# Kernel optimization log

Hardware: AMD Instinct MI355X
Metric: run time of the kernel (lower is better)

Reference implementation:

```python
import jax, jax.numpy as jnp
import numpy as np

NUM_LUT, IN_F, OUT_F = 3, 4096, 4096
VEC, LUT, GROUP = 4, 16, 128
G = IN_F // VEC            # 1024 vector-groups along in_features
NG = IN_F // GROUP         # 32 quantization groups


def setup_inputs() -> dict:
    key = jax.random.key(0)
    k1, k2, k3, k4 = jax.random.split(key, 4)
    gate = jax.random.normal(k1, (NUM_LUT, G, OUT_F, LUT), dtype=jnp.float32)
    codebook = jax.random.normal(k2, (NUM_LUT, G, LUT, VEC), dtype=jnp.float32)
    scales = jax.random.normal(k3, (OUT_F, NG), dtype=jnp.float32)
    zeros = jax.random.randint(k4, (OUT_F, NG), 0, 16, dtype=jnp.int32)
    return {"gate": gate, "codebook": codebook, "scales": scales, "zeros": zeros}


def reference(gate, codebook, scales, zeros):
    # gate: [L, G, O, S]; codebook: [L, G, S, V]
    # one-hot(argmax(gate)) @ codebook  ==  gather codebook at argmax index
    idx = jnp.argmax(gate, axis=-1)                                   # [L, G, O]
    w = jnp.take_along_axis(codebook, idx[..., None], axis=2)          # [L, G, O, V]
    w = jnp.sum(w.transpose(0, 2, 1, 3), axis=0)                       # [O, G, V]
    w = w.reshape(OUT_F, NG, GROUP)                                    # regroup (G*V == IN_F)
    w = (w - zeros.astype(w.dtype)[..., None]) * scales[..., None]     # dequantize
    return w.reshape(OUT_F, IN_F)
```

## Files before the change

### kernel.cpp

```cpp
#include <hip/hip_runtime.h>

constexpr int NUM_LUT = 3;
constexpr int IN_F    = 4096;
constexpr int OUT_F   = 4096;
constexpr int VEC     = 4;
constexpr int LUT     = 16;
constexpr int GROUP   = 128;
constexpr int G       = IN_F / VEC;
constexpr int NG      = IN_F / GROUP;

typedef float f32x4 __attribute__((ext_vector_type(4)));

constexpr int GT    = 4;
constexpr int OT    = 16;
constexpr int BLOCK = 256;

__global__ __launch_bounds__(BLOCK) void recon_kernel(
    const float* __restrict__ gate,
    const float* __restrict__ codebook,
    const float* __restrict__ scales,
    const int*   __restrict__ zeros,
    float* __restrict__ out)
{
    __shared__ __align__(16) float cb[NUM_LUT * GT * LUT * VEC];
    __shared__ float sred[OT][GT * VEC + 1];

    const int t    = threadIdx.x;
    const int w    = t >> 6;
    const int lane = t & 63;
    const int grp  = lane >> 2;
    const int c    = lane & 3;

    const int g0 = blockIdx.x * GT;
    const int o0 = blockIdx.y * OT;
    const int g  = g0 + w;
    const int o  = o0 + grp;

    if (t < NUM_LUT * GT * LUT) {
        const int l = t >> 6, rem = t & 63, gl = rem >> 4, s = rem & 15;
        reinterpret_cast<f32x4*>(cb)[t] =
            reinterpret_cast<const f32x4*>(codebook)[(l * G + g0 + gl) * LUT + s];
    }
    __syncthreads();

    f32x4 q[NUM_LUT];
    #pragma unroll
    for (int l = 0; l < NUM_LUT; ++l) {
        const float* gp = gate + ((size_t)(l * G + g) * OUT_F + o0) * LUT;
        q[l] = *reinterpret_cast<const f32x4*>(gp + lane * 4);
    }

    float acc = 0.f;
    #pragma unroll
    for (int l = 0; l < NUM_LUT; ++l) {
        float bv = q[l].x; int bi = c * 4;
        if (q[l].y > bv) { bv = q[l].y; bi = c * 4 + 1; }
        if (q[l].z > bv) { bv = q[l].z; bi = c * 4 + 2; }
        if (q[l].w > bv) { bv = q[l].w; bi = c * 4 + 3; }
        #pragma unroll
        for (int m = 1; m <= 2; m <<= 1) {
            float ov = __shfl_xor(bv, m, 64);
            int   oi = __shfl_xor(bi, m, 64);
            if (ov > bv || (ov == bv && oi < bi)) { bv = ov; bi = oi; }
        }
        acc += cb[((l * GT + w) * LUT + bi) * VEC + c];
    }

    const int   ng = g >> 5;
    const float sc = scales[o * NG + ng];
    const float zp = (float)zeros[o * NG + ng];
    const float r  = (acc - zp) * sc;

    sred[grp][w * VEC + c] = r;
    __syncthreads();

    if (t < 64) {
        const int row = t >> 2, ch = t & 3;
        f32x4 v;
        v.x = sred[row][ch * 4 + 0];
        v.y = sred[row][ch * 4 + 1];
        v.z = sred[row][ch * 4 + 2];
        v.w = sred[row][ch * 4 + 3];
        *reinterpret_cast<f32x4*>(out + (size_t)(o0 + row) * IN_F + g0 * VEC + ch * 4) = v;
    }
}

extern "C" void kernel_launch(void* const* d_in, const int* in_sizes, int n_in,
                              void* d_out, int out_size, void* d_ws, size_t ws_size,
                              hipStream_t stream) {
    const float* gate     = (const float*)d_in[0];
    const float* codebook = (const float*)d_in[1];
    const float* scales   = (const float*)d_in[2];
    const int*   zeros    = (const int*)d_in[3];
    float*       out      = (float*)d_out;

    dim3 grid(G / GT, OUT_F / OT);
    recon_kernel<<<grid, BLOCK, 0, stream>>>(gate, codebook, scales, zeros, out);
}
```

Measured before the change: 180.1 us.

## Process four output tiles per block to amortize codebook load and syncs

Each block now handles 64 output rows instead of 16, issuing 12 independent vector gate loads per thread before the argmax work. This amortizes the shared codebook staging and barriers over more outputs and gives each thread more memory parallelism. All 256 threads now take part in the final vectorized store, and shared memory is padded to allow 16-byte reads. The cost is more registers per thread and four times fewer blocks.

```diff
diff --git a/kernel.cpp b/kernel.cpp
--- a/kernel.cpp
+++ b/kernel.cpp
@@ -13,7 +13,10 @@
 
 constexpr int GT    = 4;
 constexpr int OT    = 16;
+constexpr int ITER  = 4;
+constexpr int OB    = OT * ITER;
 constexpr int BLOCK = 256;
+constexpr int PAD   = 20;
 
 __global__ __launch_bounds__(BLOCK) void recon_kernel(
     const float* __restrict__ gate,
@@ -23,7 +26,7 @@
     float* __restrict__ out)
 {
     __shared__ __align__(16) float cb[NUM_LUT * GT * LUT * VEC];
-    __shared__ float sred[OT][GT * VEC + 1];
+    __shared__ __align__(16) float sred[OB][PAD];
 
     const int t    = threadIdx.x;
     const int w    = t >> 6;
@@ -32,9 +35,8 @@
     const int c    = lane & 3;
 
     const int g0 = blockIdx.x * GT;
-    const int o0 = blockIdx.y * OT;
+    const int o0 = blockIdx.y * OB;
     const int g  = g0 + w;
-    const int o  = o0 + grp;
 
     if (t < NUM_LUT * GT * LUT) {
         const int l = t >> 6, rem = t & 63, gl = rem >> 4, s = rem & 15;
@@ -43,45 +45,49 @@
     }
     __syncthreads();
 
-    f32x4 q[NUM_LUT];
+    f32x4 q[ITER][NUM_LUT];
     #pragma unroll
-    for (int l = 0; l < NUM_LUT; ++l) {
-        const float* gp = gate + ((size_t)(l * G + g) * OUT_F + o0) * LUT;
-        q[l] = *reinterpret_cast<const f32x4*>(gp + lane * 4);
+    for (int i = 0; i < ITER; ++i) {
+        #pragma unroll
+        for (int l = 0; l < NUM_LUT; ++l) {
+            const f32x4* gp = reinterpret_cast<const f32x4*>(
+                gate + ((size_t)(l * G + g) * OUT_F + o0 + i * OT) * LUT);
+            q[i][l] = gp[lane];
+        }
     }
 
-    float acc = 0.f;
+    const int ng = g >> 5;
+
     #pragma unroll
-    for (int l = 0; l < NUM_LUT; ++l) {
-        float bv = q[l].x; int bi = c * 4;
-        if (q[l].y > bv) { bv = q[l].y; bi = c * 4 + 1; }
-        if (q[l].z > bv) { bv = q[l].z; bi = c * 4 + 2; }
-        if (q[l].w > bv) { bv = q[l].w; bi = c * 4 + 3; }
+    for (int i = 0; i < ITER; ++i) {
+        const int o = o0 + i * OT + grp;
+        float acc = 0.f;
         #pragma unroll
-        for (int m = 1; m <= 2; m <<= 1) {
-            float ov = __shfl_xor(bv, m, 64);
-            int   oi = __shfl_xor(bi, m, 64);
-            if (ov > bv || (ov == bv && oi < bi)) { bv = ov; bi = oi; }
+        for (int l = 0; l < NUM_LUT; ++l) {
+            const f32x4 v = q[i][l];
+            float bv = v.x; int bi = c * 4;
+            if (v.y > bv) { bv = v.y; bi = c * 4 + 1; }
+            if (v.z > bv) { bv = v.z; bi = c * 4 + 2; }
+            if (v.w > bv) { bv = v.w; bi = c * 4 + 3; }
+            #pragma unroll
+            for (int m = 1; m <= 2; m <<= 1) {
+                const float ov = __shfl_xor(bv, m, 64);
+                const int   oi = __shfl_xor(bi, m, 64);
+                if (ov > bv || (ov == bv && oi < bi)) { bv = ov; bi = oi; }
+            }
+            acc += cb[((l * GT + w) * LUT + bi) * VEC + c];
         }
-        acc += cb[((l * GT + w) * LUT + bi) * VEC + c];
+        const float sc = scales[o * NG + ng];
+        const float zp = (float)zeros[o * NG + ng];
+        sred[i * OT + grp][w * VEC + c] = (acc - zp) * sc;
     }
-
-    const int   ng = g >> 5;
-    const float sc = scales[o * NG + ng];
-    const float zp = (float)zeros[o * NG + ng];
-    const float r  = (acc - zp) * sc;
-
-    sred[grp][w * VEC + c] = r;
     __syncthreads();
 
-    if (t < 64) {
+    {
         const int row = t >> 2, ch = t & 3;
-        f32x4 v;
-        v.x = sred[row][ch * 4 + 0];
-        v.y = sred[row][ch * 4 + 1];
-        v.z = sred[row][ch * 4 + 2];
-        v.w = sred[row][ch * 4 + 3];
-        *reinterpret_cast<f32x4*>(out + (size_t)(o0 + row) * IN_F + g0 * VEC + ch * 4) = v;
+        const f32x4 v = *reinterpret_cast<const f32x4*>(&sred[row][ch * 4]);
+        *reinterpret_cast<f32x4*>(
+            out + (size_t)(o0 + row) * IN_F + g0 * VEC + ch * 4) = v;
     }
 }
 
@@ -94,6 +100,6 @@
     const int*   zeros    = (const int*)d_in[3];
     float*       out      = (float*)d_out;
 
-    dim3 grid(G / GT, OUT_F / OT);
+    dim3 grid(G / GT, OUT_F / OB);
     recon_kernel<<<grid, BLOCK, 0, stream>>>(gate, codebook, scales, zeros, out);
 }
```

Measured after the change: 182.2 us. Within noise of the previous version (+1.1%).
